# Optimization experiments

Measured on AMD Instinct MI355X. Metric: run time of the kernel, lower is better.

Reference implementation:

```python
import jax, jax.numpy as jnp
import numpy as np

EPS = 1e-5
HEADS = 8
GROUPS = 8
DIM_HEAD = 64
SCALE = DIM_HEAD ** -0.5
DSF = 4            # downsample_factor
OFF_SCALE = 4.0    # offset_scale
OFF_PAD = 1        # (offset_kernel_size - downsample_factor)//2


def batchnorm(x, g, b):
    # training-mode BatchNorm2d: biased batch stats over (N,H,W)
    m = x.mean(axis=(0, 2, 3), keepdims=True)
    v = x.var(axis=(0, 2, 3), keepdims=True)
    return (x - m) * jax.lax.rsqrt(v + EPS) * g[None, :, None, None] + b[None, :, None, None]


def grouped_conv1x1(x, w):
    # x: (B, G*Ci, H, W), w: (G, Co, Ci) -> (B, G*Co, H, W)
    B, C, H, W = x.shape
    G, Co, Ci = w.shape
    y = jnp.einsum('bgchw,goc->bgohw', x.reshape(B, G, Ci, H, W), w)
    return y.reshape(B, G * Co, H, W)


def conv1x1(x, w, b):
    # x: (B,C,H,W), w: (O,C), b: (O,)
    return jnp.einsum('bchw,oc->bohw', x, w) + b[None, :, None, None]


def norm_grid(h, w):
    # (h,w,2) with channel order (x,y); matches lucidrains create_grid_like+normalize_grid
    # (original normalizes x by h-1, y by w-1; identical for square maps)
    gy, gx = jnp.meshgrid(jnp.arange(h, dtype=jnp.float32), jnp.arange(w, dtype=jnp.float32), indexing='ij')
    nx = 2.0 * gx / max(h - 1, 1) - 1.0
    ny = 2.0 * gy / max(w - 1, 1) - 1.0
    return jnp.stack([nx, ny], axis=-1)


def grid_sample_bilinear(img, grid):
    # img: (N,C,H,W); grid: (N,Hg,Wg,2) with (x,y) in [-1,1]
    # mode='bilinear', padding_mode='zeros', align_corners=False (torch F.grid_sample)
    N, C, H, W = img.shape
    x = ((grid[..., 0] + 1.0) * W - 1.0) * 0.5
    y = ((grid[..., 1] + 1.0) * H - 1.0) * 0.5
    x0 = jnp.floor(x)
    y0 = jnp.floor(y)
    wx1 = x - x0
    wy1 = y - y0
    x0i = x0.astype(jnp.int32)
    y0i = y0.astype(jnp.int32)

    def gather(ix, iy):
        valid = (ix >= 0) & (ix < W) & (iy >= 0) & (iy < H)
        ixc = jnp.clip(ix, 0, W - 1)
        iyc = jnp.clip(iy, 0, H - 1)
        vals = jax.vmap(lambda im, yy, xx: im[:, yy, xx])(img, iyc, ixc)  # (N,C,Hg,Wg)
        return vals * valid[:, None, :, :].astype(img.dtype)

    v00 = gather(x0i, y0i)
    v10 = gather(x0i + 1, y0i)
    v01 = gather(x0i, y0i + 1)
    v11 = gather(x0i + 1, y0i + 1)
    wx1e = wx1[:, None]
    wy1e = wy1[:, None]
    return (v00 * (1 - wx1e) * (1 - wy1e) + v10 * wx1e * (1 - wy1e)
            + v01 * (1 - wx1e) * wy1e + v11 * wx1e * wy1e)


def deformable_attention(x, q_w, k_w, v_w, off_dw_w, off_dw_b, off_pw_w,
                         cpb_w0, cpb_b0, cpb_w1, cpb_b1, cpb_w2, cpb_b2,
                         out_w, out_b):
    B, C, H, W = x.shape
    G = GROUPS
    Cg = C // G  # offset_dims = 64

    q = grouped_conv1x1(x, q_w)  # (B,C,H,W)

    # offsets from grouped queries: depthwise 6x6 stride-4 conv -> GELU -> 1x1 -> tanh*scale
    gq = q.reshape(B * G, Cg, H, W)
    off = jax.lax.conv_general_dilated(
        gq, off_dw_w, window_strides=(DSF, DSF), padding=[(OFF_PAD, OFF_PAD)] * 2,
        feature_group_count=Cg, dimension_numbers=('NCHW', 'OIHW', 'NCHW'))
    off = off + off_dw_b[None, :, None, None]
    off = jax.nn.gelu(off, approximate=False)
    off = jnp.einsum('bchw,oc->bohw', off, off_pw_w)  # (BG,2,h2,w2)
    off = jnp.tanh(off) * OFF_SCALE
    h2, w2 = off.shape[-2:]

    # vgrid = integer grid + offsets, normalized to [-1,1] (channel order x,y)
    gy, gx = jnp.meshgrid(jnp.arange(h2, dtype=x.dtype), jnp.arange(w2, dtype=x.dtype), indexing='ij')
    vgrid = jnp.stack([gx, gy], axis=0)[None] + off  # (BG,2,h2,w2)
    vx = 2.0 * vgrid[:, 0] / max(h2 - 1, 1) - 1.0
    vy = 2.0 * vgrid[:, 1] / max(w2 - 1, 1) - 1.0
    vgrid_scaled = jnp.stack([vx, vy], axis=-1)  # (BG,h2,w2,2)

    # sample kv features at deformed locations
    kv = grid_sample_bilinear(x.reshape(B * G, Cg, H, W), vgrid_scaled)
    kv = kv.reshape(B, C, h2, w2)
    k = grouped_conv1x1(kv, k_w)
    v = grouped_conv1x1(kv, v_w)

    q = q * SCALE

    def to_heads(t):
        b, c, hh, ww = t.shape
        return t.reshape(b, HEADS, DIM_HEAD, hh * ww).transpose(0, 1, 3, 2)  # b h (hw) d

    qh, kh, vh = to_heads(q), to_heads(k), to_heads(v)
    sim = jnp.einsum('bhid,bhjd->bhij', qh, kh)  # (B,H,i=HW,j=h2*w2)

    # continuous positional bias (CPB)
    i, j = H * W, h2 * w2
    grid_q = norm_grid(H, W).reshape(i, 2)
    grid_kv = vgrid_scaled.reshape(B * G, j, 2)
    pos = grid_q[None, :, None, :] - grid_kv[:, None, :, :]  # (BG,i,j,2)
    bias = jnp.sign(pos) * jnp.log(jnp.abs(pos) + 1.0)
    bias = jax.nn.relu(bias @ cpb_w0 + cpb_b0)
    bias = jax.nn.relu(bias @ cpb_w1 + cpb_b1)
    bias = bias @ cpb_w2 + cpb_b2  # (BG,i,j,o) with o = heads//groups = 1
    o = HEADS // G
    bias = bias.reshape(B, G, i, j, o).transpose(0, 1, 4, 2, 3).reshape(B, G * o, i, j)

    attn = jax.nn.softmax(sim + bias, axis=-1)  # (max-subtract in original == stable softmax)
    out = jnp.einsum('bhij,bhjd->bhid', attn, vh)
    out = out.transpose(0, 1, 3, 2).reshape(B, HEADS * DIM_HEAD, H, W)
    return conv1x1(out, out_w, out_b)


def setup_inputs() -> dict:
    key = jax.random.key(0)
    ks = jax.random.split(key, 12)
    B, C, H, W = 2, 512, 32, 32
    G = GROUPS
    s = 0.02
    f32 = jnp.float32
    return {
        'x': jax.random.normal(ks[0], (B, C, H, W), f32),
        'n1_g': jnp.ones((C,), f32), 'n1_b': jnp.zeros((C,), f32),
        'n2_g': jnp.ones((C,), f32), 'n2_b': jnp.zeros((C,), f32),
        'q_w': jax.random.normal(ks[1], (G, C // G, C // G), f32) * s,
        'k_w': jax.random.normal(ks[2], (G, C // G, C // G), f32) * s,
        'v_w': jax.random.normal(ks[3], (G, C // G, C // G), f32) * s,
        'off_dw_w': jax.random.normal(ks[4], (C // G, 1, 6, 6), f32) * s,
        'off_dw_b': jnp.zeros((C // G,), f32),
        'off_pw_w': jax.random.normal(ks[5], (2, C // G), f32) * s,
        'cpb_w0': jax.random.normal(ks[6], (2, 128), f32) * s, 'cpb_b0': jnp.zeros((128,), f32),
        'cpb_w1': jax.random.normal(ks[7], (128, 128), f32) * s, 'cpb_b1': jnp.zeros((128,), f32),
        'cpb_w2': jax.random.normal(ks[8], (128, 1), f32) * s, 'cpb_b2': jnp.zeros((1,), f32),
        'out_w': jax.random.normal(ks[9], (C, C), f32) * s, 'out_b': jnp.zeros((C,), f32),
        'mlp_w1': jax.random.normal(ks[10], (4 * C, C), f32) * s, 'mlp_b1': jnp.zeros((4 * C,), f32),
        'mlp_w2': jax.random.normal(ks[11], (C, 4 * C), f32) * s, 'mlp_b2': jnp.zeros((C,), f32),
    }


def reference(x, n1_g, n1_b, n2_g, n2_b, q_w, k_w, v_w, off_dw_w, off_dw_b, off_pw_w,
              cpb_w0, cpb_b0, cpb_w1, cpb_b1, cpb_w2, cpb_b2, out_w, out_b,
              mlp_w1, mlp_b1, mlp_w2, mlp_b2):
    x = x + deformable_attention(batchnorm(x, n1_g, n1_b), q_w, k_w, v_w,
                                 off_dw_w, off_dw_b, off_pw_w,
                                 cpb_w0, cpb_b0, cpb_w1, cpb_b1, cpb_w2, cpb_b2,
                                 out_w, out_b)
    h = batchnorm(x, n2_g, n2_b)
    h = jax.nn.gelu(conv1x1(h, mlp_w1, mlp_b1), approximate=False)
    h = conv1x1(h, mlp_w2, mlp_b2)
    return x + h
```

## Files before the change

### kernel.cpp

```cpp
#include <hip/hip_runtime.h>
#include <cstdint>
#include <cstddef>

#define BATCH 2
#define CCH   512
#define HWPIX 1024
#define SCALE 0.125f
#define TU0  (-1.45f)
#define TDU  (2.9f/63.0f)
#define TINV (63.0f/2.9f)

typedef short bh8 __attribute__((ext_vector_type(8)));
typedef float f32x4 __attribute__((ext_vector_type(4)));
typedef unsigned short u16;
typedef u16 us8 __attribute__((ext_vector_type(8)));
typedef u16 us4 __attribute__((ext_vector_type(4)));

__device__ __forceinline__ u16 f2bf(float f){
  unsigned u = __float_as_uint(f);
  unsigned r = (u + 0x7FFFu + ((u>>16)&1u))>>16;
  return (u16)r;
}
__device__ __forceinline__ float geluf(float v){ return 0.5f*v*(1.0f + erff(v*0.70710678118654752f)); }
__device__ __forceinline__ float rdlane(float v, int l){
  return __uint_as_float(__builtin_amdgcn_readlane(__float_as_uint(v), l));
}

__global__ __launch_bounds__(256) void cvtw_kernel(
    const float* __restrict__ qw, const float* __restrict__ kw, const float* __restrict__ vw,
    const float* __restrict__ ow, const float* __restrict__ m1, const float* __restrict__ m2,
    u16* __restrict__ dst){
  int idx = (blockIdx.x*256 + threadIdx.x)*4;
  if(idx >= 2457600) return;
  const float* src; int off;
  if(idx < 32768){ src=qw; off=idx; }
  else if(idx <   65536){ src=kw; off=idx-32768; }
  else if(idx <   98304){ src=vw; off=idx-65536; }
  else if(idx <  360448){ src=ow; off=idx-98304; }
  else if(idx < 1409024){ src=m1; off=idx-360448; }
  else                  { src=m2; off=idx-1409024; }
  float4 v = *(const float4*)&src[off];
  us4 r = (us4){f2bf(v.x), f2bf(v.y), f2bf(v.z), f2bf(v.w)};
  *(us4*)&dst[idx] = r;
}

__global__ __launch_bounds__(256) void bnstat_kernel(const float* __restrict__ src,
      const float* __restrict__ g, const float* __restrict__ bta, float* __restrict__ AB){
  int c = blockIdx.x; int t = threadIdx.x;
  float s=0.f, ss=0.f;
  for(int b=0;b<BATCH;b++){
    size_t base = (size_t)b*CCH*HWPIX + (size_t)c*HWPIX;
    for(int p=t;p<HWPIX;p+=256){
      float v = src[base+p];
      s += v; ss += v*v;
    }
  }
  for(int o=32;o;o>>=1){ s += __shfl_down(s,o); ss += __shfl_down(ss,o); }
  __shared__ float ls[4], lss[4];
  int w = t>>6, lane = t&63;
  if(lane==0){ ls[w]=s; lss[w]=ss; }
  __syncthreads();
  if(t==0){
    float S=ls[0]+ls[1]+ls[2]+ls[3], SS=lss[0]+lss[1]+lss[2]+lss[3];
    float m = S*(1.0f/2048.0f);
    float var = SS*(1.0f/2048.0f) - m*m;
    float r = rsqrtf(var + 1e-5f);
    AB[c]     = r*g[c];
    AB[512+c] = bta[c] - m*r*g[c];
  }
}

__global__ __launch_bounds__(256) void bntrans_kernel(const float* __restrict__ src,
      const float* __restrict__ AB, float* __restrict__ dstF, u16* __restrict__ dstT, int tMode){
  __shared__ float tile[64*65];
  int t = threadIdx.x;
  int p0 = blockIdx.x*64, gq = blockIdx.y, b = blockIdx.z;
  int pl = t&63, seg = t>>6;
  #pragma unroll
  for(int r=0;r<16;r++){
    int c = seg*16 + r;
    int ch = gq*64 + c;
    size_t a = (size_t)b*524288 + (size_t)ch*1024 + p0 + pl;
    float v = src[a]*AB[ch] + AB[512+ch];
    tile[c*65 + pl] = v;
    if(dstF) dstF[a] = v;
  }
  __syncthreads();
  int c = t&63;
  #pragma unroll
  for(int r=0;r<16;r++){
    int p = seg*16 + r;
    float v = tile[c*65 + p];
    size_t a = tMode ? ((size_t)b*524288 + (size_t)(p0+p)*512 + gq*64 + c)
                     : ((size_t)(b*8+gq)*65536 + (size_t)(p0+p)*64 + c);
    dstT[a] = f2bf(v);
  }
}

template<int NT, int TOUT>
__global__ __launch_bounds__(256,4) void gemm_lds(
    const u16* __restrict__ W, const u16* __restrict__ Xt,
    float* __restrict__ outF, u16* __restrict__ outT,
    const float* __restrict__ bias, const float* __restrict__ resF,
    int M, int K, int Nb, int wMask, int wStride, int doGelu){
  __shared__ __align__(16) u16 xS[64*NT*64];
  __shared__ __align__(16) u16 wS[64*64];
  int t = threadIdx.x;
  int w = t>>6, lane = t&63, l15 = lane&15, quad = lane>>4;
  int n0 = blockIdx.x*(64*NT), m0 = blockIdx.y*64, batch = blockIdx.z;
  const u16* Wg = W + (size_t)(batch & wMask)*wStride + (size_t)m0*K;
  const u16* Xg = Xt + (size_t)batch*Nb*K + (size_t)n0*K;
  const u16* pX[2*NT]; u16* sX[2*NT];
  #pragma unroll
  for(int p=0;p<2*NT;p++){
    int row = (p*256 + t)>>3, kb = t&7;
    pX[p] = Xg + (size_t)row*K + kb*8;
    sX[p] = &xS[(row*8 + (kb ^ (row&7)))*8];
  }
  int row0 = t>>3,        kb0 = t&7;
  int row1 = (256+t)>>3,  kb1 = t&7;
  const u16* pW0 = Wg + (size_t)row0*K + kb0*8;
  const u16* pW1 = Wg + (size_t)row1*K + kb1*8;
  u16* sW0 = &wS[(row0*8 + (kb0 ^ (row0&7)))*8];
  u16* sW1 = &wS[(row1*8 + (kb1 ^ (row1&7)))*8];
  f32x4 acc[4][NT];
  #pragma unroll
  for(int mt=0;mt<4;mt++)
    #pragma unroll
    for(int nt=0;nt<NT;nt++) acc[mt][nt] = (f32x4){0.f,0.f,0.f,0.f};
  us8 rx[2*NT], rw0, rw1;
  #pragma unroll
  for(int p=0;p<2*NT;p++) rx[p] = *(const us8*)pX[p];
  rw0 = *(const us8*)pW0; rw1 = *(const us8*)pW1;
  for(int kc=0;kc<K;kc+=64){
    #pragma unroll
    for(int p=0;p<2*NT;p++) *(us8*)sX[p] = rx[p];
    *(us8*)sW0 = rw0;  *(us8*)sW1 = rw1;
    __syncthreads();
    if(kc+64 < K){
      #pragma unroll
      for(int p=0;p<2*NT;p++) rx[p] = *(const us8*)(pX[p] + kc+64);
      rw0 = *(const us8*)(pW0 + kc+64);  rw1 = *(const us8*)(pW1 + kc+64);
    }
    #pragma unroll
    for(int ks=0;ks<2;ks++){
      bh8 bF[NT];
      #pragma unroll
      for(int nt=0;nt<NT;nt++){
        int rb = (w*NT + nt)*16 + l15;
        bF[nt] = *(const bh8*)&xS[rb*64 + ((ks*4+quad) ^ (rb&7))*8];
      }
      #pragma unroll
      for(int mt=0;mt<4;mt++){
        int ra = mt*16 + l15;
        bh8 aF = *(const bh8*)&wS[ra*64 + ((ks*4+quad) ^ (ra&7))*8];
        #pragma unroll
        for(int nt=0;nt<NT;nt++)
          acc[mt][nt] = __builtin_amdgcn_mfma_f32_16x16x32_bf16(aF, bF[nt], acc[mt][nt], 0,0,0);
      }
    }
    __syncthreads();
  }
  if(TOUT){
    size_t oB = (size_t)batch*Nb*(size_t)M;
    #pragma unroll
    for(int nt=0;nt<NT;nt++){
      int n = n0 + (w*NT + nt)*16 + l15;
      #pragma unroll
      for(int mt=0;mt<4;mt++){
        int m = m0 + mt*16 + quad*4;
        us4 pk;
        #pragma unroll
        for(int reg=0;reg<4;reg++){
          float v = acc[mt][nt][reg];
          if(bias) v += bias[m+reg];
          if(doGelu) v = geluf(v);
          pk[reg] = f2bf(v);
        }
        *(us4*)&outT[oB + (size_t)n*M + m] = pk;
      }
    }
  } else {
    size_t oB = (size_t)batch*(size_t)M*Nb;
    #pragma unroll
    for(int nt=0;nt<NT;nt++){
      int n = n0 + (w*NT + nt)*16 + l15;
      #pragma unroll
      for(int mt=0;mt<4;mt++)
        #pragma unroll
        for(int reg=0;reg<4;reg++){
          int m = m0 + mt*16 + quad*4 + reg;
          float v = acc[mt][nt][reg];
          if(bias) v += bias[m];
          if(doGelu) v = geluf(v);
          size_t a = oB + (size_t)m*Nb + n;
          if(resF) v += resF[a];
          outF[a] = v;
        }
    }
  }
}

__global__ __launch_bounds__(256) void dwconv_kernel(const float* __restrict__ q,
    const float* __restrict__ dw, const float* __restrict__ dwb, float* __restrict__ offg){
  int t = threadIdx.x;
  int bgc = blockIdx.x*4 + (t>>6);
  int c = bgc & 63;
  int pix = t&63;
  int oy = pix>>3, ox = pix&7;
  const float* img = q + (size_t)bgc*HWPIX;
  float acc = dwb[c];
  #pragma unroll
  for(int ky=0;ky<6;ky++){
    int y = oy*4 - 1 + ky;
    if(y<0 || y>31) continue;
    #pragma unroll
    for(int kx=0;kx<6;kx++){
      int x = ox*4 - 1 + kx;
      if(x<0 || x>31) continue;
      acc = fmaf(img[y*32 + x], dw[c*36 + ky*6 + kx], acc);
    }
  }
  offg[(size_t)bgc*64 + pix] = geluf(acc);
}

__global__ __launch_bounds__(64) void pwgrid_kernel(const float* __restrict__ offg,
    const float* __restrict__ pw, float* __restrict__ vgrid){
  int bg = blockIdx.x; int p = threadIdx.x;
  float a0=0.f, a1=0.f;
  for(int c=0;c<64;c++){
    float v = offg[(size_t)bg*4096 + c*64 + p];
    a0 = fmaf(v, pw[c], a0);
    a1 = fmaf(v, pw[64+c], a1);
  }
  float o0 = tanhf(a0)*4.0f, o1 = tanhf(a1)*4.0f;
  float gx = (float)(p&7), gy = (float)(p>>3);
  float vxx = (2.0f/7.0f)*(gx + o0) - 1.0f;
  float vyy = (2.0f/7.0f)*(gy + o1) - 1.0f;
  vgrid[bg*128 + p*2]     = vxx;
  vgrid[bg*128 + p*2 + 1] = vyy;
}

__device__ __forceinline__ float fetchpix(const float* img, int ix, int iy){
  return (ix>=0 && ix<32 && iy>=0 && iy<32) ? img[iy*32+ix] : 0.0f;
}
__global__ __launch_bounds__(256) void sample_kernel(const float* __restrict__ xn,
    const float* __restrict__ vgrid, u16* __restrict__ kvT){
  int bg = blockIdx.x; int t = threadIdx.x;
  int p = t&63, cblk = t>>6;
  int cbase = blockIdx.y*16 + cblk*4;
  float vx = vgrid[bg*128 + p*2], vy = vgrid[bg*128 + p*2+1];
  float xs = ((vx + 1.0f)*32.0f - 1.0f)*0.5f;
  float ys = ((vy + 1.0f)*32.0f - 1.0f)*0.5f;
  float x0 = floorf(xs), y0 = floorf(ys);
  float wx = xs - x0, wy = ys - y0;
  int ix0 = (int)x0, iy0 = (int)y0;
  int b = bg>>3, g = bg&7;
  float w00 = (1.f-wx)*(1.f-wy), w10 = wx*(1.f-wy), w01 = (1.f-wx)*wy, w11 = wx*wy;
  us4 tmp;
  #pragma unroll
  for(int cc=0;cc<4;cc++){
    int c = cbase + cc;
    const float* img = xn + (size_t)b*CCH*HWPIX + (size_t)(g*64+c)*HWPIX;
    float acc = w00*fetchpix(img,ix0,iy0)   + w10*fetchpix(img,ix0+1,iy0)
              + w01*fetchpix(img,ix0,iy0+1) + w11*fetchpix(img,ix0+1,iy0+1);
    tmp[cc] = f2bf(acc);
  }
  *(us4*)&kvT[(size_t)bg*4096 + p*64 + cbase] = tmp;
}

__global__ __launch_bounds__(256) void tabbuild_kernel(
    const float* __restrict__ w0, const float* __restrict__ b0,
    const float* __restrict__ w1, const float* __restrict__ b1,
    const float* __restrict__ w2, const float* __restrict__ b2,
    float* __restrict__ tab){
  int t = threadIdx.x;
  int eloc = t & 15, chunk = t >> 4;
  int e = blockIdx.x*16 + eloc;
  int iu = e & 63, iv = e >> 6;
  float u = TU0 + iu*TDU, v = TU0 + iv*TDU;
  float acc[8] = {0.f,0.f,0.f,0.f,0.f,0.f,0.f,0.f};
  for(int k=0;k<128;k++){
    float h0 = fmaxf(fmaf(u, w0[k], fmaf(v, w0[128+k], b0[k])), 0.f);
    const float* wr = &w1[k*128 + chunk*8];
    #pragma unroll
    for(int n=0;n<8;n++) acc[n] = fmaf(h0, wr[n], acc[n]);
  }
  float partial = 0.f;
  #pragma unroll
  for(int n=0;n<8;n++)
    partial = fmaf(fmaxf(acc[n] + b1[chunk*8+n], 0.f), w2[chunk*8+n], partial);
  __shared__ float red[16][17];
  red[eloc][chunk] = partial;
  __syncthreads();
  if(chunk==0){
    float s = b2[0];
    #pragma unroll
    for(int c2=0;c2<16;c2++) s += red[eloc][c2];
    tab[e] = s;
  }
}

__global__ __launch_bounds__(256) void biaseval_kernel(
    const float* __restrict__ vgrid, const float* __restrict__ tab,
    float* __restrict__ biasOut){
  int t = threadIdx.x;
  int bg = blockIdx.x >> 6, jj = blockIdx.x & 63;
  float vx = vgrid[bg*128 + jj*2];
  float vy = vgrid[bg*128 + jj*2 + 1];
  int i0 = t*4;
  int gy = i0 >> 5, gx0 = i0 & 31;
  float py = (2.0f/31.0f)*(float)gy - 1.0f - vy;
  float v = copysignf(__logf(1.0f + fabsf(py)), py);
  float fv = (v - TU0) * TINV;
  int iv = (int)floorf(fv);
  iv = iv < 0 ? 0 : (iv > 62 ? 62 : iv);
  fv -= (float)iv;
  f32x4 res;
  #pragma unroll
  for(int c=0;c<4;c++){
    float px = (2.0f/31.0f)*(float)(gx0 + c) - 1.0f - vx;
    float u = copysignf(__logf(1.0f + fabsf(px)), px);
    float fu = (u - TU0) * TINV;
    int iu = (int)floorf(fu);
    iu = iu < 0 ? 0 : (iu > 62 ? 62 : iu);
    fu -= (float)iu;
    const float* p0 = &tab[iv*64 + iu];
    const float* p1 = p0 + 64;
    float a = fmaf(fu, p0[1] - p0[0], p0[0]);
    float b = fmaf(fu, p1[1] - p1[0], p1[0]);
    res[c] = fmaf(fv, b - a, a);
  }
  *(f32x4*)&biasOut[(size_t)bg*65536 + (size_t)jj*1024 + i0] = res;
}

__global__ __launch_bounds__(256) void attn_kernel(
    const float* __restrict__ qb, const float* __restrict__ kb, const float* __restrict__ vb,
    const float* __restrict__ biasb, u16* __restrict__ obT){
  __shared__ float qT[64*65], kT[64*65], vT[64*65], bT[64*65];
  int t = threadIdx.x;
  int bg = blockIdx.x>>4, itile = blockIdx.x&15;
  int i0 = itile*64;
  size_t qBase = (size_t)bg*65536;
  for(int e=t;e<4096;e+=256){
    int d = e>>6, x = e&63;
    qT[d*65 + x] = qb[qBase + (size_t)d*HWPIX + i0 + x];
    kT[d*65 + x] = kb[(size_t)bg*4096 + e];
    vT[d*65 + x] = vb[(size_t)bg*4096 + e];
    bT[x*65 + d] = biasb[(size_t)bg*65536 + (size_t)d*1024 + i0 + x];
  }
  __syncthreads();
  int lane = t&63, w = t>>6;
  int b = bg>>3, g = bg&7;
  for(int rr=0;rr<16;rr++){
    int il = w*16 + rr;
    int i = i0 + il;
    float qreg = qT[lane*65 + il];
    float s0=0.f,s1=0.f,s2=0.f,s3=0.f;
    #pragma unroll 4
    for(int d=0;d<64;d+=4){
      s0 = fmaf(rdlane(qreg,d  ), kT[(d  )*65 + lane], s0);
      s1 = fmaf(rdlane(qreg,d+1), kT[(d+1)*65 + lane], s1);
      s2 = fmaf(rdlane(qreg,d+2), kT[(d+2)*65 + lane], s2);
      s3 = fmaf(rdlane(qreg,d+3), kT[(d+3)*65 + lane], s3);
    }
    float s = (s0+s1)+(s2+s3);
    s = s*SCALE + bT[il*65 + lane];
    float m = s;
    for(int msk=32;msk;msk>>=1) m = fmaxf(m, __shfl_xor(m, msk));
    float p = __expf(s - m);
    float l = p;
    for(int msk=32;msk;msk>>=1) l += __shfl_xor(l, msk);
    p = p / l;
    float o0=0.f,o1=0.f,o2=0.f,o3=0.f;
    #pragma unroll 4
    for(int j=0;j<64;j+=4){
      o0 = fmaf(rdlane(p,j  ), vT[lane*65 + j  ], o0);
      o1 = fmaf(rdlane(p,j+1), vT[lane*65 + j+1], o1);
      o2 = fmaf(rdlane(p,j+2), vT[lane*65 + j+2], o2);
      o3 = fmaf(rdlane(p,j+3), vT[lane*65 + j+3], o3);
    }
    obT[(size_t)b*524288 + (size_t)i*512 + g*64 + lane] = f2bf((o0+o1)+(o2+o3));
  }
}

extern "C" void kernel_launch(void* const* d_in, const int* in_sizes, int n_in,
                              void* d_out, int out_size, void* d_ws, size_t ws_size,
                              hipStream_t stream){
  const float* x    = (const float*)d_in[0];
  const float* n1g  = (const float*)d_in[1];
  const float* n1b  = (const float*)d_in[2];
  const float* n2g  = (const float*)d_in[3];
  const float* n2b  = (const float*)d_in[4];
  const float* qw   = (const float*)d_in[5];
  const float* kw   = (const float*)d_in[6];
  const float* vw   = (const float*)d_in[7];
  const float* dww  = (const float*)d_in[8];
  const float* dwb  = (const float*)d_in[9];
  const float* pww  = (const float*)d_in[10];
  const float* cw0  = (const float*)d_in[11];
  const float* cb0  = (const float*)d_in[12];
  const float* cw1  = (const float*)d_in[13];
  const float* cb1  = (const float*)d_in[14];
  const float* cw2  = (const float*)d_in[15];
  const float* cb2  = (const float*)d_in[16];
  const float* ow   = (const float*)d_in[17];
  const float* obb  = (const float*)d_in[18];
  const float* m1w  = (const float*)d_in[19];
  const float* m1bi = (const float*)d_in[20];
  const float* m2w  = (const float*)d_in[21];
  const float* m2bi = (const float*)d_in[22];
  float* out = (float*)d_out;
  float* ws = (float*)d_ws;

  float* xn     = ws;
  float* x2     = ws + 1048576;
  float* q      = ws + 2097152;
  float* biasb  = ws + 3145728;
  u16*   hT     = (u16*)(ws + 2097152);
  u16*   attnT  = (u16*)(ws + 4194304);
  u16*   xnT    = (u16*)(ws + 4718592);
  u16*   kvT    = (u16*)(ws + 5242880);
  float* tab    = ws + 5242880;
  float* kbuf   = ws + 5275648;
  float* vbuf   = ws + 5341184;
  float* offg   = ws + 5406720;
  float* bnAB   = offg;
  float* vgrid  = ws + 5472256;
  u16*   wbf    = (u16*)(ws + 5474304);
  u16 *qwb = wbf, *kwb = wbf+32768, *vwb = wbf+65536, *owb = wbf+98304;
  u16 *m1wb = wbf+360448, *m2wb = wbf+1409024;

  cvtw_kernel<<<2400,256,0,stream>>>(qw,kw,vw,ow,m1w,m2w,wbf);
  bnstat_kernel<<<512,256,0,stream>>>(x, n1g, n1b, bnAB);
  bntrans_kernel<<<dim3(16,8,2),256,0,stream>>>(x, bnAB, xn, xnT, 0);
  gemm_lds<1,0><<<dim3(16,1,16),256,0,stream>>>(qwb, xnT, q, nullptr, nullptr, nullptr,
                                                64,64,1024, 7, 4096, 0);
  dwconv_kernel<<<256,256,0,stream>>>(q, dww, dwb, offg);
  pwgrid_kernel<<<16,64,0,stream>>>(offg, pww, vgrid);
  sample_kernel<<<dim3(16,4),256,0,stream>>>(xn, vgrid, kvT);
  gemm_lds<1,0><<<dim3(1,1,16),256,0,stream>>>(kwb, kvT, kbuf, nullptr, nullptr, nullptr,
                                               64,64,64, 7, 4096, 0);
  gemm_lds<1,0><<<dim3(1,1,16),256,0,stream>>>(vwb, kvT, vbuf, nullptr, nullptr, nullptr,
                                               64,64,64, 7, 4096, 0);
  tabbuild_kernel<<<256,256,0,stream>>>(cw0, cb0, cw1, cb1, cw2, cb2, tab);
  biaseval_kernel<<<1024,256,0,stream>>>(vgrid, tab, biasb);
  attn_kernel<<<256,256,0,stream>>>(q, kbuf, vbuf, biasb, attnT);
  gemm_lds<1,0><<<dim3(16,8,2),256,0,stream>>>(owb, attnT, x2, nullptr, obb, x,
                                               512,512,1024, 0,0,0);
  bnstat_kernel<<<512,256,0,stream>>>(x2, n2g, n2b, bnAB);
  bntrans_kernel<<<dim3(16,8,2),256,0,stream>>>(x2, bnAB, nullptr, xnT, 1);
  gemm_lds<2,1><<<dim3(8,32,2),256,0,stream>>>(m1wb, xnT, nullptr, hT, m1bi, nullptr,
                                               2048,512,1024, 0,0,1);
  gemm_lds<1,0><<<dim3(16,8,2),256,0,stream>>>(m2wb, hT, out, nullptr, m2bi, x2,
                                               512,2048,1024, 0,0,0);
}
```

Before: 250.1 us.

## Move attention QK and PV products onto bf16 MFMA with transposed bf16 Q/K

The attention kernel is rewritten to compute the QK^T scores and the P·V product with 16x16x32 bf16 MFMA instructions instead of scalar FMAs driven by readlane broadcasts. The Q projection GEMM gains a dual-output epilogue that writes fp32 Q for the offset conv plus a pre-scaled, transposed bf16 copy. The K projection now emits transposed bf16 directly. This removes the scalar inner loops and the fp32 shared-memory transposes, at the cost of bf16 rounding of Q, K, V and the probabilities, plus an extra write of Q.

```diff
diff --git a/kernel.cpp b/kernel.cpp
--- a/kernel.cpp
+++ b/kernel.cpp
@@ -22,9 +22,6 @@
   return (u16)r;
 }
 __device__ __forceinline__ float geluf(float v){ return 0.5f*v*(1.0f + erff(v*0.70710678118654752f)); }
-__device__ __forceinline__ float rdlane(float v, int l){
-  return __uint_as_float(__builtin_amdgcn_readlane(__float_as_uint(v), l));
-}
 
 __global__ __launch_bounds__(256) void cvtw_kernel(
     const float* __restrict__ qw, const float* __restrict__ kw, const float* __restrict__ vw,
@@ -161,7 +158,7 @@
     }
     __syncthreads();
   }
-  if(TOUT){
+  if(TOUT==1){
     size_t oB = (size_t)batch*Nb*(size_t)M;
     #pragma unroll
     for(int nt=0;nt<NT;nt++){
@@ -178,6 +175,25 @@
           pk[reg] = f2bf(v);
         }
         *(us4*)&outT[oB + (size_t)n*M + m] = pk;
+      }
+    }
+  } else if(TOUT==2){
+    size_t oBF = (size_t)batch*(size_t)M*Nb;
+    size_t oBT = (size_t)batch*Nb*(size_t)M;
+    #pragma unroll
+    for(int nt=0;nt<NT;nt++){
+      int n = n0 + (w*NT + nt)*16 + l15;
+      #pragma unroll
+      for(int mt=0;mt<4;mt++){
+        int m = m0 + mt*16 + quad*4;
+        us4 pk;
+        #pragma unroll
+        for(int reg=0;reg<4;reg++){
+          float v = acc[mt][nt][reg];
+          outF[oBF + (size_t)(m+reg)*Nb + n] = v;
+          pk[reg] = f2bf(v*SCALE);
+        }
+        *(us4*)&outT[oBT + (size_t)n*M + m] = pk;
       }
     }
   } else {
@@ -335,53 +351,93 @@
 }
 
 __global__ __launch_bounds__(256) void attn_kernel(
-    const float* __restrict__ qb, const float* __restrict__ kb, const float* __restrict__ vb,
+    const u16* __restrict__ qTb, const u16* __restrict__ kTb, const float* __restrict__ vb,
     const float* __restrict__ biasb, u16* __restrict__ obT){
-  __shared__ float qT[64*65], kT[64*65], vT[64*65], bT[64*65];
+  __shared__ __align__(16) u16 qS[64*64], kS[64*64];
+  __shared__ __align__(16) u16 vS[64*72], pS[64*72];
   int t = threadIdx.x;
+  int w = t>>6, lane = t&63, l15 = lane&15, quad = lane>>4;
   int bg = blockIdx.x>>4, itile = blockIdx.x&15;
   int i0 = itile*64;
-  size_t qBase = (size_t)bg*65536;
+  #pragma unroll
+  for(int p=0;p<2;p++){
+    int idx = p*256 + t;
+    int row = idx>>3, kb = t&7;
+    int sw = ((kb ^ (row&7)))*8;
+    *(us8*)&qS[row*64 + sw] = *(const us8*)&qTb[(size_t)bg*65536 + (size_t)(i0+row)*64 + kb*8];
+    *(us8*)&kS[row*64 + sw] = *(const us8*)&kTb[(size_t)bg*4096  + (size_t)row*64      + kb*8];
+  }
   for(int e=t;e<4096;e+=256){
-    int d = e>>6, x = e&63;
-    qT[d*65 + x] = qb[qBase + (size_t)d*HWPIX + i0 + x];
-    kT[d*65 + x] = kb[(size_t)bg*4096 + e];
-    vT[d*65 + x] = vb[(size_t)bg*4096 + e];
-    bT[x*65 + d] = biasb[(size_t)bg*65536 + (size_t)d*1024 + i0 + x];
+    int d = e>>6, j = e&63;
+    vS[d*72 + j] = f2bf(vb[(size_t)bg*4096 + e]);
   }
   __syncthreads();
-  int lane = t&63, w = t>>6;
+  f32x4 sAcc[4];
+  #pragma unroll
+  for(int jt=0;jt<4;jt++){
+    int jg = jt*16 + l15;
+    sAcc[jt] = *(const f32x4*)&biasb[(size_t)bg*65536 + (size_t)jg*1024 + i0 + w*16 + quad*4];
+  }
+  int ra = w*16 + l15;
+  #pragma unroll
+  for(int ks=0;ks<2;ks++){
+    bh8 aF = *(const bh8*)&qS[ra*64 + ((ks*4+quad) ^ (ra&7))*8];
+    #pragma unroll
+    for(int jt=0;jt<4;jt++){
+      int rb = jt*16 + l15;
+      bh8 bF = *(const bh8*)&kS[rb*64 + ((ks*4+quad) ^ (rb&7))*8];
+      sAcc[jt] = __builtin_amdgcn_mfma_f32_16x16x32_bf16(aF, bF, sAcc[jt], 0,0,0);
+    }
+  }
+  #pragma unroll
+  for(int reg=0;reg<4;reg++){
+    float m = fmaxf(fmaxf(sAcc[0][reg], sAcc[1][reg]), fmaxf(sAcc[2][reg], sAcc[3][reg]));
+    m = fmaxf(m, __shfl_xor(m, 1));
+    m = fmaxf(m, __shfl_xor(m, 2));
+    m = fmaxf(m, __shfl_xor(m, 4));
+    m = fmaxf(m, __shfl_xor(m, 8));
+    float li = 0.f;
+    #pragma unroll
+    for(int jt=0;jt<4;jt++){
+      float e = __expf(sAcc[jt][reg] - m);
+      sAcc[jt][reg] = e;
+      li += e;
+    }
+    li += __shfl_xor(li, 1);
+    li += __shfl_xor(li, 2);
+    li += __shfl_xor(li, 4);
+    li += __shfl_xor(li, 8);
+    float inv = 1.0f / li;
+    #pragma unroll
+    for(int jt=0;jt<4;jt++) sAcc[jt][reg] *= inv;
+  }
+  #pragma unroll
+  for(int jt=0;jt<4;jt++)
+    #pragma unroll
+    for(int reg=0;reg<4;reg++)
+      pS[(w*16 + quad*4 + reg)*72 + jt*16 + l15] = f2bf(sAcc[jt][reg]);
+  __syncthreads();
+  f32x4 oAcc[4];
+  #pragma unroll
+  for(int dt=0;dt<4;dt++) oAcc[dt] = (f32x4){0.f,0.f,0.f,0.f};
+  int rp = w*16 + l15;
+  #pragma unroll
+  for(int ks=0;ks<2;ks++){
+    bh8 aP = *(const bh8*)&pS[rp*72 + ks*32 + quad*8];
+    #pragma unroll
+    for(int dt=0;dt<4;dt++){
+      bh8 bV = *(const bh8*)&vS[(dt*16 + l15)*72 + ks*32 + quad*8];
+      oAcc[dt] = __builtin_amdgcn_mfma_f32_16x16x32_bf16(aP, bV, oAcc[dt], 0,0,0);
+    }
+  }
   int b = bg>>3, g = bg&7;
-  for(int rr=0;rr<16;rr++){
-    int il = w*16 + rr;
-    int i = i0 + il;
-    float qreg = qT[lane*65 + il];
-    float s0=0.f,s1=0.f,s2=0.f,s3=0.f;
-    #pragma unroll 4
-    for(int d=0;d<64;d+=4){
-      s0 = fmaf(rdlane(qreg,d  ), kT[(d  )*65 + lane], s0);
-      s1 = fmaf(rdlane(qreg,d+1), kT[(d+1)*65 + lane], s1);
-      s2 = fmaf(rdlane(qreg,d+2), kT[(d+2)*65 + lane], s2);
-      s3 = fmaf(rdlane(qreg,d+3), kT[(d+3)*65 + lane], s3);
-    }
-    float s = (s0+s1)+(s2+s3);
-    s = s*SCALE + bT[il*65 + lane];
-    float m = s;
-    for(int msk=32;msk;msk>>=1) m = fmaxf(m, __shfl_xor(m, msk));
-    float p = __expf(s - m);
-    float l = p;
-    for(int msk=32;msk;msk>>=1) l += __shfl_xor(l, msk);
-    p = p / l;
-    float o0=0.f,o1=0.f,o2=0.f,o3=0.f;
-    #pragma unroll 4
-    for(int j=0;j<64;j+=4){
-      o0 = fmaf(rdlane(p,j  ), vT[lane*65 + j  ], o0);
-      o1 = fmaf(rdlane(p,j+1), vT[lane*65 + j+1], o1);
-      o2 = fmaf(rdlane(p,j+2), vT[lane*65 + j+2], o2);
-      o3 = fmaf(rdlane(p,j+3), vT[lane*65 + j+3], o3);
-    }
-    obT[(size_t)b*524288 + (size_t)i*512 + g*64 + lane] = f2bf((o0+o1)+(o2+o3));
-  }
+  #pragma unroll
+  for(int dt=0;dt<4;dt++)
+    #pragma unroll
+    for(int reg=0;reg<4;reg++){
+      int i = i0 + w*16 + quad*4 + reg;
+      obT[(size_t)b*524288 + (size_t)i*512 + g*64 + dt*16 + l15] = f2bf(oAcc[dt][reg]);
+    }
 }
 
 extern "C" void kernel_launch(void* const* d_in, const int* in_sizes, int n_in,
@@ -422,30 +478,31 @@
   u16*   xnT    = (u16*)(ws + 4718592);
   u16*   kvT    = (u16*)(ws + 5242880);
   float* tab    = ws + 5242880;
-  float* kbuf   = ws + 5275648;
+  u16*   kTb    = (u16*)(ws + 5275648);
   float* vbuf   = ws + 5341184;
   float* offg   = ws + 5406720;
   float* bnAB   = offg;
   float* vgrid  = ws + 5472256;
   u16*   wbf    = (u16*)(ws + 5474304);
+  u16*   qTb    = (u16*)(ws + 6703104);
   u16 *qwb = wbf, *kwb = wbf+32768, *vwb = wbf+65536, *owb = wbf+98304;
   u16 *m1wb = wbf+360448, *m2wb = wbf+1409024;
 
   cvtw_kernel<<<2400,256,0,stream>>>(qw,kw,vw,ow,m1w,m2w,wbf);
   bnstat_kernel<<<512,256,0,stream>>>(x, n1g, n1b, bnAB);
   bntrans_kernel<<<dim3(16,8,2),256,0,stream>>>(x, bnAB, xn, xnT, 0);
-  gemm_lds<1,0><<<dim3(16,1,16),256,0,stream>>>(qwb, xnT, q, nullptr, nullptr, nullptr,
+  gemm_lds<1,2><<<dim3(16,1,16),256,0,stream>>>(qwb, xnT, q, qTb, nullptr, nullptr,
                                                 64,64,1024, 7, 4096, 0);
   dwconv_kernel<<<256,256,0,stream>>>(q, dww, dwb, offg);
   pwgrid_kernel<<<16,64,0,stream>>>(offg, pww, vgrid);
   sample_kernel<<<dim3(16,4),256,0,stream>>>(xn, vgrid, kvT);
-  gemm_lds<1,0><<<dim3(1,1,16),256,0,stream>>>(kwb, kvT, kbuf, nullptr, nullptr, nullptr,
+  gemm_lds<1,1><<<dim3(1,1,16),256,0,stream>>>(kwb, kvT, nullptr, kTb, nullptr, nullptr,
                                                64,64,64, 7, 4096, 0);
   gemm_lds<1,0><<<dim3(1,1,16),256,0,stream>>>(vwb, kvT, vbuf, nullptr, nullptr, nullptr,
                                                64,64,64, 7, 4096, 0);
   tabbuild_kernel<<<256,256,0,stream>>>(cw0, cb0, cw1, cb1, cw2, cb2, tab);
   biaseval_kernel<<<1024,256,0,stream>>>(vgrid, tab, biasb);
-  attn_kernel<<<256,256,0,stream>>>(q, kbuf, vbuf, biasb, attnT);
+  attn_kernel<<<256,256,0,stream>>>(qTb, kTb, vbuf, biasb, attnT);
   gemm_lds<1,0><<<dim3(16,8,2),256,0,stream>>>(owb, attnT, x2, nullptr, obb, x,
                                                512,512,1024, 0,0,0);
   bnstat_kernel<<<512,256,0,stream>>>(x2, n2g, n2b, bnAB);
```

Measured after the change: 218.7 us. -12.5%, faster.
